# Optimization experiments

Hardware: AMD Instinct MI355X
Metric: run time of the kernel (lower is better)

Reference implementation:

```python
import jax, jax.numpy as jnp
import numpy as np

N_SAMPLES = 256   # n_samples from __init__
N_THIN = 10       # N from __init__
N_WORDS = 4096


def setup_inputs() -> dict:
    key = jax.random.key(0)
    k1, k2, k3 = jax.random.split(key, 3)
    # scale potentials so per-step weight deltas stay in a sane exp() range
    bigram = jax.random.normal(k1, (N_WORDS, N_WORDS), dtype=jnp.float32)
    start = jax.random.normal(k2, (N_WORDS,), dtype=jnp.float32)
    end = jax.random.normal(k3, (N_WORDS,), dtype=jnp.float32)
    return {"n_words": N_WORDS, "bigram": bigram, "start": start, "end": end}


def _mh_chain(bigram, start, end, n_words, chain_size, rng):
    # chain[0] = identity permutation (random_start=False)
    perm0 = jnp.arange(n_words, dtype=jnp.int32)
    w0 = bigram[perm0[:-1], perm0[1:]].sum() + start[perm0[0]] + end[perm0[-1]]

    def step(carry, k):
        perm, w_last = carry
        k_pos, k_cat, k_u = jax.random.split(k, 3)
        # pick a token to move, remove it -> perm2 of length n_words-1
        pos = jax.random.randint(k_pos, (), 0, n_words)
        to_move = perm[pos]
        j = jnp.arange(n_words - 1)
        perm2 = perm[j + (j >= pos).astype(j.dtype)]
        # insertion logits over n_words slots (self._probs, unnormalized log p)
        logits = jnp.zeros((n_words,), dtype=bigram.dtype)
        logits = logits.at[0].add(start[to_move]).at[-1].add(end[to_move])
        logits = logits.at[1:].add(bigram[perm2, to_move])   # left-neighbor term
        logits = logits.at[:-1].add(bigram[to_move, perm2])  # right-neighbor term
        p = jax.nn.softmax(logits)
        new_pos = jax.random.categorical(k_cat, logits)
        # insert to_move at new_pos
        jj = jnp.arange(n_words)
        shifted = perm2[jnp.clip(jj - (jj > new_pos).astype(jj.dtype), 0, n_words - 2)]
        sample = jnp.where(jj == new_pos, to_move, shifted).astype(perm.dtype)
        # new chain weight
        new_w = bigram[sample[:-1], sample[1:]].sum() + start[sample[0]] + end[sample[-1]]
        # MH accept ratio; removing to_move from sample recovers perm2, so the
        # reverse insertion distribution equals p -> ratio p[new_pos]/p[pos]
        acc = jnp.minimum(1.0, jnp.exp(new_w - w_last) * p[new_pos] / p[pos])
        accept = acc > jax.random.uniform(k_u, ())
        perm_next = jnp.where(accept, sample, perm)
        w_next = jnp.where(accept, new_w, w_last)
        return (perm_next, w_next), perm_next

    keys = jax.random.split(rng, chain_size - 1)
    _, perms = jax.lax.scan(step, (perm0, w0), keys)
    chain = jnp.concatenate([perm0[None, :], perms], axis=0)  # [chain_size, n_words]
    sel = jnp.arange(0, chain_size, N_THIN) + (N_THIN - 1)    # thin: every N-th state
    return chain[sel]


def reference(n_words, bigram, start, end):
    chain_size = N_SAMPLES * N_THIN
    rng = jax.random.key(42)
    return _mh_chain(bigram, start, end, n_words, chain_size, rng)
```

## Files before the change

### kernel.cpp

```cpp
#include <hip/hip_runtime.h>
#include <stdint.h>


#define NW 4096
#define NSTEPS 2559
#define NTHREADS 1024
#define NWAVES 16

typedef unsigned long long u64;
typedef uint32_t u32;
typedef unsigned short u16;

__device__ __forceinline__ u32 rotl32(u32 v, u32 r) { return (v << r) | (v >> (32u - r)); }

__device__ __forceinline__ void tf2x32(u32 k0, u32 k1, u32 x0, u32 x1, u32* o0, u32* o1) {
  u32 ks2 = k0 ^ k1 ^ 0x1BD11BDAu;
  x0 += k0; x1 += k1;
#define TFR(r0, r1, r2, r3)                      \
  x0 += x1; x1 = rotl32(x1, r0); x1 ^= x0;       \
  x0 += x1; x1 = rotl32(x1, r1); x1 ^= x0;       \
  x0 += x1; x1 = rotl32(x1, r2); x1 ^= x0;       \
  x0 += x1; x1 = rotl32(x1, r3); x1 ^= x0;
  TFR(13, 15, 26, 6)  x0 += k1;  x1 += ks2 + 1u;
  TFR(17, 29, 16, 24) x0 += ks2; x1 += k0 + 2u;
  TFR(13, 15, 26, 6)  x0 += k0;  x1 += k1 + 3u;
  TFR(17, 29, 16, 24) x0 += k1;  x1 += ks2 + 4u;
  TFR(13, 15, 26, 6)  x0 += ks2; x1 += k0 + 5u;
#undef TFR
  *o0 = x0; *o1 = x1;
}

__device__ __forceinline__ float unif01(u32 bits) {
  return __uint_as_float((bits >> 9) | 0x3f800000u) - 1.0f;
}

__device__ __forceinline__ u32 fkey(float f) {
  u32 b = __float_as_uint(f);
  return b ^ ((b >> 31) ? 0xFFFFFFFFu : 0x80000000u);
}

__device__ __forceinline__ void light_bar() {
  asm volatile("s_waitcnt lgkmcnt(0)" ::: "memory");
  __builtin_amdgcn_s_barrier();
  __builtin_amdgcn_sched_barrier(0);
  asm volatile("" ::: "memory");
}


template <int CTRL>
__device__ __forceinline__ u32 dpp32(u32 v) {
  return (u32)__builtin_amdgcn_update_dpp(0, (int)v, CTRL, 0xF, 0xF, true);
}

template <int CTRL>
__device__ __forceinline__ u32 dppumax(u32 v) {
  u32 s = dpp32<CTRL>(v);
  return (v > s) ? v : s;
}

template <int CTRL>
__device__ __forceinline__ void dppmax64(u32& hi, u32& lo) {
  u32 h2 = dpp32<CTRL>(hi);
  u32 l2 = dpp32<CTRL>(lo);
  bool g = (h2 > hi) || (h2 == hi && l2 > lo);
  hi = g ? h2 : hi;
  lo = g ? l2 : lo;
}

__device__ __forceinline__ u64 bfly16_max_u64(u64 key) {
  u32 lo = (u32)key, hi = (u32)(key >> 32);
  dppmax64<0xB1>(hi, lo); dppmax64<0x4E>(hi, lo);
  dppmax64<0x141>(hi, lo); dppmax64<0x140>(hi, lo);
  return ((u64)hi << 32) | lo;
}


#define TT 32
__global__ void transpose_k(const float* __restrict__ in, float* __restrict__ out) {
  __shared__ float tile[TT][TT + 1];
  int x = blockIdx.x * TT + threadIdx.x;
  int y = blockIdx.y * TT + threadIdx.y;
  for (int j = 0; j < TT; j += 8) tile[threadIdx.y + j][threadIdx.x] = in[(u64)(y + j) * NW + x];
  __syncthreads();
  x = blockIdx.y * TT + threadIdx.x;
  y = blockIdx.x * TT + threadIdx.y;
  for (int j = 0; j < TT; j += 8) out[(u64)(y + j) * NW + x] = tile[threadIdx.x][threadIdx.y + j];
}

__global__ void gumbel_k(float* __restrict__ gumb) {
  long long idx = (long long)blockIdx.x * blockDim.x + threadIdx.x;
  if (idx >= (long long)NSTEPS * NW) return;
  int t = (int)(idx >> 12);
  int i = (int)(idx & (NW - 1));
  u32 kt0, kt1, kc0, kc1, ba, bb;
  tf2x32(0u, 42u, 0u, (u32)t, &kt0, &kt1);
  tf2x32(kt0, kt1, 0u, 1u, &kc0, &kc1);
  tf2x32(kc0, kc1, 0u, (u32)i, &ba, &bb);
  float u = unif01(ba ^ bb);
  if (u == 0.0f) u = 1.17549435e-38f;
  float t1 = (float)log((double)u);
  float t2 = (float)log((double)(-t1));
  gumb[idx] = -t2;
}

__global__ void posu_k(int* __restrict__ posArr, float* __restrict__ uArr) {
  int t = blockIdx.x * blockDim.x + threadIdx.x;
  if (t >= NSTEPS) return;
  u32 kt0, kt1, kp0, kp1, ku0, ku1, k2a, k2b, ra, rb, ua, ub;
  tf2x32(0u, 42u, 0u, (u32)t, &kt0, &kt1);
  tf2x32(kt0, kt1, 0u, 0u, &kp0, &kp1);
  tf2x32(kt0, kt1, 0u, 2u, &ku0, &ku1);
  tf2x32(kp0, kp1, 0u, 1u, &k2a, &k2b);
  tf2x32(k2a, k2b, 0u, 0u, &ra, &rb);
  posArr[t] = (int)((ra ^ rb) & (u32)(NW - 1));
  tf2x32(ku0, ku1, 0u, 0u, &ua, &ub);
  uArr[t] = unif01(ua ^ ub);
}


#define SAMPLE_AT(idx)                                                        \
  ((idx) < np ? (int)s_perm[(idx) + ((idx) >= pos)]                           \
              : ((idx) == np ? tm                                             \
                             : (int)s_perm[((idx)-1) + (((idx)-1) >= pos)]))

__global__ __launch_bounds__(NTHREADS)
void mcmc_fast16(const float* __restrict__ bigram,
                 const float* __restrict__ bigT,
                 const float* __restrict__ gumb,
                 const int* __restrict__ posArr,
                 const float* __restrict__ uArr,
                 const float* __restrict__ startv,
                 const float* __restrict__ endv,
                 int* __restrict__ out) {
  __shared__ u16    s_perm[NW];
  __shared__ float  s_rowT[NW];
  __shared__ float  s_rowB[NW];
  __shared__ float  s_pairw[NW];
  __shared__ u64    s_redu[NWAVES];
  __shared__ float  s_stm, s_etm, s_lpos, s_brgS, s_vn1, s_vn2;
  __shared__ int    s_accs, s_tmA;

  const int tid = threadIdx.x;
  const int lane = tid & 63;
  const int wid = tid >> 6;
  const int j0 = tid * 4;

  for (int i = tid; i < NW; i += NTHREADS) s_perm[i] = (u16)i;
  ushort4 pq = make_ushort4((u16)j0, (u16)(j0 + 1), (u16)(j0 + 2), (u16)(j0 + 3));
  float4 pwq;
  pwq.x = bigram[(u64)j0 * NW + (j0 + 1)];
  pwq.y = bigram[(u64)(j0 + 1) * NW + (j0 + 2)];
  pwq.z = bigram[(u64)(j0 + 2) * NW + (j0 + 3)];
  pwq.w = (j0 + 3 < NW - 1) ? bigram[(u64)(j0 + 3) * NW + (j0 + 4)] : 0.0f;
  ((float4*)s_pairw)[tid] = pwq;

  int pos = posArr[0];
  int pn1 = posArr[1];
  float u_cur = uArr[0];
  float un1 = uArr[1];
  int tm = pos;
  {
    float4 rb4 = ((const float4*)(bigram + (u64)tm * NW))[tid];
    float4 rt4 = ((const float4*)(bigT + (u64)tm * NW))[tid];
    ((float4*)s_rowB)[tid] = rb4;
    ((float4*)s_rowT)[tid] = rt4;
  }
  if (tid == 0) { s_stm = startv[tm]; s_etm = endv[tm]; }

  float start_cur = startv[0];
  float end_cur = endv[NW - 1];

  float4 g4 = ((const float4*)gumb)[tid];
  __syncthreads();

  for (int t = 0; t < NSTEPS; ++t) {
    const float gg[4] = {g4.x, g4.y, g4.z, g4.w};
    const int tmR = (int)s_perm[pn1];
    const float4 rbR = ((const float4*)(bigram + (u64)tmR * NW))[tid];
    const float4 rtR = ((const float4*)(bigT + (u64)tmR * NW))[tid];
    float stmR = 0.0f, etmR = 0.0f;
    if (tid == 0) { stmR = startv[tmR]; etmR = endv[tmR]; }
    int pn2; float un2;
    {
      int tn = (t + 1 < NSTEPS) ? (t + 1) : (NSTEPS - 1);
      int tn2 = (t + 2 < NSTEPS) ? (t + 2) : (NSTEPS - 1);
      g4 = ((const float4*)(gumb + ((u64)tn << 12)))[tid];
      pn2 = posArr[tn2];
      un2 = uArr[tn2];
    }
    float stm_r = 0.0f, etm_r = 0.0f, remL = 0.0f, remR = 0.0f, brgv = 0.0f;
    float sv0m = 0.0f, ev1m = 0.0f;
    if (wid == 0) {
      stm_r = s_stm; etm_r = s_etm;
      int pl = (pos > 0) ? (int)s_perm[pos - 1] : 0;
      int pr = (pos < NW - 1) ? (int)s_perm[pos + 1] : 0;
      if (pos > 0)      remL = s_rowT[pl];
      if (pos < NW - 1) remR = s_rowB[pr];
      if (pos > 0 && pos < NW - 1) brgv = bigram[(u64)pl * NW + pr];
      sv0m = startv[(int)s_perm[(0 >= pos) ? 1 : 0]];
      ev1m = endv[(int)s_perm[(NW - 2) + ((NW - 2) >= pos)]];
      if (lane == 0) s_brgS = brgv;
    }

    const int p0i = pq.x, p1i = pq.y, p2i = pq.z, p3i = pq.w;
    int pm1, pp4;
    {
      u32 lo = (u32)pq.x | ((u32)pq.y << 16);
      u32 hi = (u32)pq.z | ((u32)pq.w << 16);
      pm1 = (int)(dpp32<0x138>(hi) >> 16);
      pp4 = (int)(dpp32<0x130>(lo) & 0xFFFFu);
      if (lane == 0)  pm1 = (tid > 0) ? (int)s_perm[j0 - 1] : 0;
      if (lane == 63) pp4 = (tid < NTHREADS - 1) ? (int)s_perm[j0 + 4] : 0;
    }
    float pwm1_e = 0.0f, pwp4_e = 0.0f;
    if (lane == 0 && tid > 0) pwm1_e = s_pairw[j0 - 1];
    if (lane == 63 && tid < NTHREADS - 1) pwp4_e = s_pairw[j0 + 4];

    const int w0 = (j0     >= pos) ? p1i : p0i;
    const int w1 = (j0 + 1 >= pos) ? p2i : p1i;
    const int w2 = (j0 + 2 >= pos) ? p3i : p2i;
    const int w3 = (j0 + 3 >= pos) ? pp4 : p3i;
    const int wprev = ((j0 - 1) >= pos) ? p0i : pm1;
    const float t0v = s_rowT[w0];
    const float t1v = s_rowT[w1];
    const float t2v = s_rowT[w2];
    const float t3v = s_rowT[w3];
    const float b0v = s_rowB[w0];
    const float b1v = s_rowB[w1];
    const float b2v = s_rowB[w2];
    const float b3v = s_rowB[w3];
    float tprev = __uint_as_float(dpp32<0x138>(__float_as_uint(t3v)));
    if (lane == 0 && tid > 0) tprev = s_rowT[wprev];
    float li0 = tprev + b0v;
    float li1 = t0v + b1v;
    float li2 = t1v + b2v;
    float li3 = t2v + b3v;
    if (tid == 0)            li0 = s_stm + b0v;
    if (tid == NTHREADS - 1) li3 = s_etm + t2v;
    if ((pos >> 2) == tid) {
      int k = pos & 3;
      s_lpos = (k == 0) ? li0 : ((k == 1) ? li1 : ((k == 2) ? li2 : li3));
    }
    {
      float sv0_ = gg[0] + li0;
      float sv1_ = gg[1] + li1;
      float sv2_ = gg[2] + li2;
      float sv3_ = gg[3] + li3;
      float mx = sv0_; int ix = j0;
      if (sv1_ > mx) { mx = sv1_; ix = j0 + 1; }
      if (sv2_ > mx) { mx = sv2_; ix = j0 + 2; }
      if (sv3_ > mx) { mx = sv3_; ix = j0 + 3; }
      u32 kloc = fkey(mx);
      u32 kr = kloc;
      kr = dppumax<0x111>(kr); kr = dppumax<0x112>(kr);
      kr = dppumax<0x114>(kr); kr = dppumax<0x118>(kr);
      kr = dppumax<0x142>(kr); kr = dppumax<0x143>(kr);
      u32 kmax = (u32)__builtin_amdgcn_readlane((int)kr, 63);
      u64 mask = __ballot(kloc == kmax);
      int wl = (int)(__ffsll((long long)mask)) - 1;
      if (lane == wl) s_redu[wid] = ((u64)kmax << 32) | (u32)(NW - 1 - ix);
    }
    light_bar();

    if (wid == 0) {
      u64 bb = bfly16_max_u64(s_redu[lane & 15]);
      const int np = NW - 1 - (int)(bb & 0xFFFFFFFFu);
      int ls_i = (np >= 1) ? ((np - 1) + ((np - 1) >= pos)) : 0;
      int rs_i = (np <= NW - 2) ? (np + (np >= pos)) : 0;
      const int l_s = (int)s_perm[ls_i];
      const int r_s = (int)s_perm[rs_i];
      const int tmA = SAMPLE_AT(pn1);
      float splitv = 0.0f;
      if (np > 0 && np < NW - 1) {
        int k_s = (np - 1) + ((np - 1) >= pos);
        splitv = (np == pos) ? brgv : s_pairw[k_s];
      }
      float vnpm1 = (np >= 1)      ? s_rowT[l_s] : 0.0f;
      float vnp   = (np <= NW - 2) ? s_rowB[r_s] : 0.0f;
      float sv0 = (np > 0) ? sv0m : stm_r;
      float ev1 = (np < NW - 1) ? ev1m : etm_r;
      float lposv = s_lpos;
      double delta = 0.0;
      if (pos > 0)                 delta -= (double)remL;
      if (pos < NW - 1)            delta -= (double)remR;
      if (pos > 0 && pos < NW - 1) delta += (double)brgv;
      if (np > 0)                  delta += (double)vnpm1;
      if (np < NW - 1)             delta += (double)vnp;
      if (np > 0 && np < NW - 1)   delta -= (double)splitv;
      delta += ((double)sv0 - (double)start_cur) + ((double)ev1 - (double)end_cur);
      float lnp = (np == 0) ? (stm_r + vnp)
                : ((np == NW - 1) ? (etm_r + vnpm1) : (vnpm1 + vnp));
      double ed = delta + ((double)lnp - (double)lposv);
      float a = fminf(1.0f, expf((float)ed));
      int acc = (a > u_cur) ? 1 : 0;
      if (lane == 0) { s_accs = acc; s_vn1 = vnpm1; s_vn2 = vnp; s_tmA = tmA; }
      if (acc) { start_cur = sv0; end_cur = ev1; }
    }
    light_bar();

    const int acc = s_accs;
    int tm_next = tmR;
    float4 rb = rbR, rt = rtR;
    ushort4 st = pq;
    if (acc) {
      tm_next = s_tmA;
      rb = ((const float4*)(bigram + (u64)tm_next * NW))[tid];
      rt = ((const float4*)(bigT + (u64)tm_next * NW))[tid];
      u64 bb = bfly16_max_u64(s_redu[lane & 15]);
      const int np = NW - 1 - (int)(bb & 0xFFFFFFFFu);
      st.x = (j0     < np) ? (u16)w0 : ((j0     == np) ? (u16)tm : (u16)wprev);
      st.y = (j0 + 1 < np) ? (u16)w1 : ((j0 + 1 == np) ? (u16)tm : (u16)w0);
      st.z = (j0 + 2 < np) ? (u16)w2 : ((j0 + 2 == np) ? (u16)tm : (u16)w1);
      st.w = (j0 + 3 < np) ? (u16)w3 : ((j0 + 3 == np) ? (u16)tm : (u16)w2);
      ((ushort4*)s_perm)[tid] = st;
      float pwm1 = __uint_as_float(dpp32<0x138>(__float_as_uint(pwq.w)));
      float pwp4 = __uint_as_float(dpp32<0x130>(__float_as_uint(pwq.x)));
      if (lane == 0)  pwm1 = pwm1_e;
      if (lane == 63) pwp4 = pwp4_e;
      const float brgAll = s_brgS;
      float nv0, nv1, nv2, nv3;
      {
        float vA0 = (j0     < pos - 1) ? pwq.x : pwq.y;
        float vB0 = (j0 - 1 < pos - 1) ? pwm1  : pwq.x;
        nv0 = (j0 < np) ? vA0 : vB0;
        int kk0 = (j0 < np) ? j0 : j0 - 1;
        if (kk0 == pos - 1) nv0 = brgAll;

        float vA1 = (j0 + 1 < pos - 1) ? pwq.y : pwq.z;
        float vB1 = (j0     < pos - 1) ? pwq.x : pwq.y;
        nv1 = (j0 + 1 < np) ? vA1 : vB1;
        int kk1 = (j0 + 1 < np) ? j0 + 1 : j0;
        if (kk1 == pos - 1) nv1 = brgAll;

        float vA2 = (j0 + 2 < pos - 1) ? pwq.z : pwq.w;
        float vB2 = (j0 + 1 < pos - 1) ? pwq.y : pwq.z;
        nv2 = (j0 + 2 < np) ? vA2 : vB2;
        int kk2 = (j0 + 2 < np) ? j0 + 2 : j0 + 1;
        if (kk2 == pos - 1) nv2 = brgAll;

        float vA3 = (j0 + 3 < pos - 1) ? pwq.w : pwp4;
        float vB3 = (j0 + 2 < pos - 1) ? pwq.z : pwq.w;
        nv3 = (j0 + 3 < np) ? vA3 : vB3;
        int kk3 = (j0 + 3 < np) ? j0 + 3 : j0 + 2;
        if (kk3 == pos - 1) nv3 = brgAll;
      }
      const float vn1 = s_vn1, vn2 = s_vn2;
      float o0 = (j0     == np - 1) ? vn1 : ((j0     == np) ? vn2 : nv0);
      float o1 = (j0 + 1 == np - 1) ? vn1 : ((j0 + 1 == np) ? vn2 : nv1);
      float o2 = (j0 + 2 == np - 1) ? vn1 : ((j0 + 2 == np) ? vn2 : nv2);
      float o3 = (j0 + 3 == np - 1) ? vn1 : ((j0 + 3 == np) ? vn2 : nv3);
      if (j0 + 3 >= NW - 1) o3 = 0.0f;
      pwq = make_float4(o0, o1, o2, o3);
      ((float4*)s_pairw)[tid] = pwq;
      if (tid == 0) { s_stm = startv[tm_next]; s_etm = endv[tm_next]; }
    } else {
      if (tid == 0) { s_stm = stmR; s_etm = etmR; }
    }
    ((float4*)s_rowB)[tid] = rb;
    ((float4*)s_rowT)[tid] = rt;
    pq = st;
    tm = tm_next;
    pos = pn1; u_cur = un1;
    pn1 = pn2; un1 = un2;

    if ((t % 10) == 8) {
      int row = (t - 8) / 10;
      int4 o4;
      o4.x = (int)pq.x; o4.y = (int)pq.y; o4.z = (int)pq.z; o4.w = (int)pq.w;
      ((int4*)(out + (u64)row * NW))[tid] = o4;
    }
    light_bar();
  }
}


__global__ __launch_bounds__(NTHREADS)
void mcmc_kernel(const float* __restrict__ bigram,
                 const float* __restrict__ startv,
                 const float* __restrict__ endv,
                 int* __restrict__ out) {
  __shared__ int    s_perm[NW];
  __shared__ float  s_logit[NW];
  __shared__ float  s_gath[NW];
  __shared__ float  s_redf[NWAVES];
  __shared__ u64    s_redu[NWAVES];
  __shared__ double s_redd[NWAVES];
  __shared__ float  s_m, s_Z, s_w;
  __shared__ int    s_pos, s_tm, s_np, s_acc;
  __shared__ u32    s_kcat0, s_kcat1, s_ku0, s_ku1;

  const int tid = threadIdx.x;
  const int lane = tid & 63;
  const int wid = tid >> 6;

  for (int i = tid; i < NW; i += NTHREADS) s_perm[i] = i;
  for (int j = tid; j < NW - 1; j += NTHREADS) s_gath[j] = bigram[(u64)j * NW + (j + 1)];
  __syncthreads();
  if (tid == 0) {
    float S = 0.0f;
    for (int j = 0; j < NW - 1; ++j) S += s_gath[j];
    S = S + startv[0];
    S = S + endv[NW - 1];
    s_w = S;
  }
  __syncthreads();

  for (int t = 0; t < NSTEPS; ++t) {
    if (tid == 0) {
      u32 kt0, kt1;
      tf2x32(0u, 42u, 0u, (u32)t, &kt0, &kt1);
      u32 kp0, kp1, kc0, kc1, ku0, ku1;
      tf2x32(kt0, kt1, 0u, 0u, &kp0, &kp1);
      tf2x32(kt0, kt1, 0u, 1u, &kc0, &kc1);
      tf2x32(kt0, kt1, 0u, 2u, &ku0, &ku1);
      u32 k2a, k2b, ra, rb;
      tf2x32(kp0, kp1, 0u, 1u, &k2a, &k2b);
      tf2x32(k2a, k2b, 0u, 0u, &ra, &rb);
      int pos = (int)((ra ^ rb) & (u32)(NW - 1));
      s_pos = pos;
      s_tm = s_perm[pos];
      s_kcat0 = kc0; s_kcat1 = kc1; s_ku0 = ku0; s_ku1 = ku1;
    }
    __syncthreads();
    const int pos = s_pos, tm = s_tm;

    float lmax = -3.402823466e+38f;
    for (int i = tid; i < NW; i += NTHREADS) {
      float li;
      if (i == 0) {
        int r = s_perm[(0 >= pos) ? 1 : 0];
        li = startv[tm] + bigram[(u64)tm * NW + r];
      } else if (i == NW - 1) {
        int l = s_perm[((NW - 2) >= pos) ? (NW - 1) : (NW - 2)];
        li = endv[tm] + bigram[(u64)l * NW + tm];
      } else {
        int l = s_perm[((i - 1) >= pos) ? i : (i - 1)];
        int r = s_perm[(i >= pos) ? (i + 1) : i];
        li = bigram[(u64)l * NW + tm] + bigram[(u64)tm * NW + r];
      }
      s_logit[i] = li;
      lmax = fmaxf(lmax, li);
    }
    for (int o = 32; o > 0; o >>= 1) lmax = fmaxf(lmax, __shfl_down(lmax, o, 64));
    if (lane == 0) s_redf[wid] = lmax;
    __syncthreads();
    if (tid == 0) {
      float m = s_redf[0];
      for (int w = 1; w < NWAVES; ++w) m = fmaxf(m, s_redf[w]);
      s_m = m;
    }
    __syncthreads();
    const float m = s_m;

    double zacc = 0.0;
    u64 best = 0;
    const u32 kc0 = s_kcat0, kc1 = s_kcat1;
    for (int i = tid; i < NW; i += NTHREADS) {
      float li = s_logit[i];
      float ex = (float)exp((double)(li - m));
      zacc += (double)ex;
      u32 ba, bb;
      tf2x32(kc0, kc1, 0u, (u32)i, &ba, &bb);
      float u = unif01(ba ^ bb);
      if (u == 0.0f) u = 1.17549435e-38f;
      float t1 = (float)log((double)u);
      float t2 = (float)log((double)(-t1));
      float g = -t2;
      float sv = g + li;
      u64 key = ((u64)fkey(sv) << 32) | (u32)(NW - 1 - i);
      if (key > best) best = key;
    }
    for (int o = 32; o > 0; o >>= 1) {
      u64 w = __shfl_down(best, o, 64);
      if (w > best) best = w;
      zacc += __shfl_down(zacc, o, 64);
    }
    if (lane == 0) { s_redu[wid] = best; s_redd[wid] = zacc; }
    __syncthreads();
    if (tid == 0) {
      u64 b = s_redu[0]; double z = s_redd[0];
      for (int w = 1; w < NWAVES; ++w) {
        if (s_redu[w] > b) b = s_redu[w];
        z += s_redd[w];
      }
      s_np = NW - 1 - (int)(b & 0xFFFFFFFFu);
      s_Z = (float)z;
    }
    __syncthreads();
    const int np = s_np;

    for (int j = tid; j < NW - 1; j += NTHREADS) {
      int a = (j < np) ? s_perm[j + (j >= pos)]
                       : ((j == np) ? tm : s_perm[(j - 1) + ((j - 1) >= pos)]);
      int j1 = j + 1;
      int b = (j1 < np) ? s_perm[j1 + (j1 >= pos)]
                        : ((j1 == np) ? tm : s_perm[(j1 - 1) + ((j1 - 1) >= pos)]);
      s_gath[j] = bigram[(u64)a * NW + b];
    }
    __syncthreads();

    if (tid == 0) {
      float S = 0.0f;
      for (int j = 0; j < NW - 1; ++j) S += s_gath[j];
      int s0 = (0 < np) ? s_perm[(0 >= pos) ? 1 : 0] : tm;
      int sl = ((NW - 1) == np) ? tm : s_perm[(NW - 2) + ((NW - 2) >= pos)];
      S = S + startv[s0];
      S = S + endv[sl];
      float dw = S - s_w;
      float e1 = (float)exp((double)dw);
      float en = (float)exp((double)(s_logit[np] - m));
      float eo = (float)exp((double)(s_logit[pos] - m));
      float pn = en / s_Z;
      float po = eo / s_Z;
      float acc = e1 * pn;
      acc = acc / po;
      acc = fminf(1.0f, acc);
      u32 ua, ub;
      tf2x32(s_ku0, s_ku1, 0u, 0u, &ua, &ub);
      float u = unif01(ua ^ ub);
      int accept = (acc > u) ? 1 : 0;
      s_acc = accept;
      if (accept) s_w = S;
    }
    __syncthreads();

    int stash[4];
    if (s_acc) {
      for (int k = 0; k < 4; ++k) {
        int i = tid + k * NTHREADS;
        stash[k] = (i < np) ? s_perm[i + (i >= pos)]
                            : ((i == np) ? tm : s_perm[(i - 1) + ((i - 1) >= pos)]);
      }
    }
    __syncthreads();
    if (s_acc) {
      for (int k = 0; k < 4; ++k) {
        int i = tid + k * NTHREADS;
        s_perm[i] = stash[k];
      }
    }
    __syncthreads();

    if (((t + 1) % 10) == 9) {
      int row = (t - 8) / 10;
      for (int i = tid; i < NW; i += NTHREADS) out[(u64)row * NW + i] = s_perm[i];
    }
    __syncthreads();
  }
}

extern "C" void kernel_launch(void* const* d_in, const int* in_sizes, int n_in,
                              void* d_out, int out_size, void* d_ws, size_t ws_size,
                              hipStream_t stream) {
  const float* bigram = (const float*)d_in[1];
  const float* startv = (const float*)d_in[2];
  const float* endv   = (const float*)d_in[3];
  int* out = (int*)d_out;

  const size_t needT = (size_t)NW * NW * sizeof(float);
  const size_t needG = (size_t)NSTEPS * NW * sizeof(float);
  const size_t needP = (size_t)NSTEPS * (sizeof(int) + sizeof(float));

  if (ws_size >= needT + needG + needP) {
    float* bigT = (float*)d_ws;
    float* gumb = (float*)((char*)d_ws + needT);
    int* posArr = (int*)((char*)d_ws + needT + needG);
    float* uArr = (float*)((char*)d_ws + needT + needG + (size_t)NSTEPS * sizeof(int));
    hipLaunchKernelGGL(transpose_k, dim3(NW / TT, NW / TT), dim3(TT, 8), 0, stream,
                       bigram, bigT);
    long long ng = (long long)NSTEPS * NW;
    hipLaunchKernelGGL(gumbel_k, dim3((unsigned)((ng + 255) / 256)), dim3(256), 0, stream,
                       gumb);
    hipLaunchKernelGGL(posu_k, dim3((NSTEPS + 255) / 256), dim3(256), 0, stream,
                       posArr, uArr);
    hipLaunchKernelGGL(mcmc_fast16, dim3(1), dim3(NTHREADS), 0, stream,
                       bigram, bigT, gumb, posArr, uArr, startv, endv, out);
  } else {
    hipLaunchKernelGGL(mcmc_kernel, dim3(1), dim3(NTHREADS), 0, stream,
                       bigram, startv, endv, out);
  }
}
```

Before: 6.496 ms.

## Double-buffer gathered row tiles and skip end-of-step barrier on reject

Splits the shared bigram row/column buffers into two copies that alternate each step. The speculative next row is written into the spare buffer right after the mid-step barrier, and the trailing barrier now runs only when a proposal is accepted and the buffers must be overwritten. The start/end potentials for the moved token also move from shared scalars into per-thread registers. Together these aim to drop one block-wide barrier per step on the common reject path, in exchange for twice the shared memory for rows and more complex ordering reasoning around buffer reuse.

```diff
diff --git a/kernel.cpp b/kernel.cpp
--- a/kernel.cpp
+++ b/kernel.cpp
@@ -124,7 +124,7 @@
                              : (int)s_perm[((idx)-1) + (((idx)-1) >= pos)]))
 
 __global__ __launch_bounds__(NTHREADS)
-void mcmc_fast16(const float* __restrict__ bigram,
+void mcmc_fast17(const float* __restrict__ bigram,
                  const float* __restrict__ bigT,
                  const float* __restrict__ gumb,
                  const int* __restrict__ posArr,
@@ -133,17 +133,18 @@
                  const float* __restrict__ endv,
                  int* __restrict__ out) {
   __shared__ u16    s_perm[NW];
-  __shared__ float  s_rowT[NW];
-  __shared__ float  s_rowB[NW];
+  __shared__ float  s_rowT[2][NW];
+  __shared__ float  s_rowB[2][NW];
   __shared__ float  s_pairw[NW];
   __shared__ u64    s_redu[NWAVES];
-  __shared__ float  s_stm, s_etm, s_lpos, s_brgS, s_vn1, s_vn2;
+  __shared__ float  s_lpos, s_brgS, s_vn1, s_vn2;
   __shared__ int    s_accs, s_tmA;
 
   const int tid = threadIdx.x;
   const int lane = tid & 63;
   const int wid = tid >> 6;
   const int j0 = tid * 4;
+  int cur = 0;
 
   for (int i = tid; i < NW; i += NTHREADS) s_perm[i] = (u16)i;
   ushort4 pq = make_ushort4((u16)j0, (u16)(j0 + 1), (u16)(j0 + 2), (u16)(j0 + 3));
@@ -162,11 +163,11 @@
   {
     float4 rb4 = ((const float4*)(bigram + (u64)tm * NW))[tid];
     float4 rt4 = ((const float4*)(bigT + (u64)tm * NW))[tid];
-    ((float4*)s_rowB)[tid] = rb4;
-    ((float4*)s_rowT)[tid] = rt4;
+    ((float4*)s_rowB[0])[tid] = rb4;
+    ((float4*)s_rowT[0])[tid] = rt4;
   }
-  if (tid == 0) { s_stm = startv[tm]; s_etm = endv[tm]; }
-
+  float stm_cur = startv[tm];
+  float etm_cur = endv[tm];
   float start_cur = startv[0];
   float end_cur = endv[NW - 1];
 
@@ -174,12 +175,15 @@
   __syncthreads();
 
   for (int t = 0; t < NSTEPS; ++t) {
+    const float* rowT = s_rowT[cur];
+    const float* rowB = s_rowB[cur];
+
     const float gg[4] = {g4.x, g4.y, g4.z, g4.w};
     const int tmR = (int)s_perm[pn1];
     const float4 rbR = ((const float4*)(bigram + (u64)tmR * NW))[tid];
     const float4 rtR = ((const float4*)(bigT + (u64)tmR * NW))[tid];
-    float stmR = 0.0f, etmR = 0.0f;
-    if (tid == 0) { stmR = startv[tmR]; etmR = endv[tmR]; }
+    const float stmR = startv[tmR];
+    const float etmR = endv[tmR];
     int pn2; float un2;
     {
       int tn = (t + 1 < NSTEPS) ? (t + 1) : (NSTEPS - 1);
@@ -188,14 +192,12 @@
       pn2 = posArr[tn2];
       un2 = uArr[tn2];
     }
-    float stm_r = 0.0f, etm_r = 0.0f, remL = 0.0f, remR = 0.0f, brgv = 0.0f;
-    float sv0m = 0.0f, ev1m = 0.0f;
+    float remL = 0.0f, remR = 0.0f, brgv = 0.0f, sv0m = 0.0f, ev1m = 0.0f;
     if (wid == 0) {
-      stm_r = s_stm; etm_r = s_etm;
       int pl = (pos > 0) ? (int)s_perm[pos - 1] : 0;
       int pr = (pos < NW - 1) ? (int)s_perm[pos + 1] : 0;
-      if (pos > 0)      remL = s_rowT[pl];
-      if (pos < NW - 1) remR = s_rowB[pr];
+      if (pos > 0)      remL = rowT[pl];
+      if (pos < NW - 1) remR = rowB[pr];
       if (pos > 0 && pos < NW - 1) brgv = bigram[(u64)pl * NW + pr];
       sv0m = startv[(int)s_perm[(0 >= pos) ? 1 : 0]];
       ev1m = endv[(int)s_perm[(NW - 2) + ((NW - 2) >= pos)]];
@@ -221,22 +223,22 @@
     const int w2 = (j0 + 2 >= pos) ? p3i : p2i;
     const int w3 = (j0 + 3 >= pos) ? pp4 : p3i;
     const int wprev = ((j0 - 1) >= pos) ? p0i : pm1;
-    const float t0v = s_rowT[w0];
-    const float t1v = s_rowT[w1];
-    const float t2v = s_rowT[w2];
-    const float t3v = s_rowT[w3];
-    const float b0v = s_rowB[w0];
-    const float b1v = s_rowB[w1];
-    const float b2v = s_rowB[w2];
-    const float b3v = s_rowB[w3];
+    const float t0v = rowT[w0];
+    const float t1v = rowT[w1];
+    const float t2v = rowT[w2];
+    const float t3v = rowT[w3];
+    const float b0v = rowB[w0];
+    const float b1v = rowB[w1];
+    const float b2v = rowB[w2];
+    const float b3v = rowB[w3];
     float tprev = __uint_as_float(dpp32<0x138>(__float_as_uint(t3v)));
-    if (lane == 0 && tid > 0) tprev = s_rowT[wprev];
+    if (lane == 0 && tid > 0) tprev = rowT[wprev];
     float li0 = tprev + b0v;
     float li1 = t0v + b1v;
     float li2 = t1v + b2v;
     float li3 = t2v + b3v;
-    if (tid == 0)            li0 = s_stm + b0v;
-    if (tid == NTHREADS - 1) li3 = s_etm + t2v;
+    if (tid == 0)            li0 = stm_cur + b0v;
+    if (tid == NTHREADS - 1) li3 = etm_cur + t2v;
     if ((pos >> 2) == tid) {
       int k = pos & 3;
       s_lpos = (k == 0) ? li0 : ((k == 1) ? li1 : ((k == 2) ? li2 : li3));
@@ -262,6 +264,8 @@
     }
     light_bar();
 
+    ((float4*)s_rowB[cur ^ 1])[tid] = rbR;
+    ((float4*)s_rowT[cur ^ 1])[tid] = rtR;
     if (wid == 0) {
       u64 bb = bfly16_max_u64(s_redu[lane & 15]);
       const int np = NW - 1 - (int)(bb & 0xFFFFFFFFu);
@@ -275,10 +279,10 @@
         int k_s = (np - 1) + ((np - 1) >= pos);
         splitv = (np == pos) ? brgv : s_pairw[k_s];
       }
-      float vnpm1 = (np >= 1)      ? s_rowT[l_s] : 0.0f;
-      float vnp   = (np <= NW - 2) ? s_rowB[r_s] : 0.0f;
-      float sv0 = (np > 0) ? sv0m : stm_r;
-      float ev1 = (np < NW - 1) ? ev1m : etm_r;
+      float vnpm1 = (np >= 1)      ? rowT[l_s] : 0.0f;
+      float vnp   = (np <= NW - 2) ? rowB[r_s] : 0.0f;
+      float sv0 = (np > 0) ? sv0m : stm_cur;
+      float ev1 = (np < NW - 1) ? ev1m : etm_cur;
       float lposv = s_lpos;
       double delta = 0.0;
       if (pos > 0)                 delta -= (double)remL;
@@ -288,8 +292,8 @@
       if (np < NW - 1)             delta += (double)vnp;
       if (np > 0 && np < NW - 1)   delta -= (double)splitv;
       delta += ((double)sv0 - (double)start_cur) + ((double)ev1 - (double)end_cur);
-      float lnp = (np == 0) ? (stm_r + vnp)
-                : ((np == NW - 1) ? (etm_r + vnpm1) : (vnpm1 + vnp));
+      float lnp = (np == 0) ? (stm_cur + vnp)
+                : ((np == NW - 1) ? (etm_cur + vnpm1) : (vnpm1 + vnp));
       double ed = delta + ((double)lnp - (double)lposv);
       float a = fminf(1.0f, expf((float)ed));
       int acc = (a > u_cur) ? 1 : 0;
@@ -300,12 +304,14 @@
 
     const int acc = s_accs;
     int tm_next = tmR;
-    float4 rb = rbR, rt = rtR;
+    float stmN = stmR, etmN = etmR;
     ushort4 st = pq;
     if (acc) {
       tm_next = s_tmA;
-      rb = ((const float4*)(bigram + (u64)tm_next * NW))[tid];
-      rt = ((const float4*)(bigT + (u64)tm_next * NW))[tid];
+      const float4 rbA = ((const float4*)(bigram + (u64)tm_next * NW))[tid];
+      const float4 rtA = ((const float4*)(bigT + (u64)tm_next * NW))[tid];
+      stmN = startv[tm_next];
+      etmN = endv[tm_next];
       u64 bb = bfly16_max_u64(s_redu[lane & 15]);
       const int np = NW - 1 - (int)(bb & 0xFFFFFFFFu);
       st.x = (j0     < np) ? (u16)w0 : ((j0     == np) ? (u16)tm : (u16)wprev);
@@ -352,16 +358,16 @@
       if (j0 + 3 >= NW - 1) o3 = 0.0f;
       pwq = make_float4(o0, o1, o2, o3);
       ((float4*)s_pairw)[tid] = pwq;
-      if (tid == 0) { s_stm = startv[tm_next]; s_etm = endv[tm_next]; }
-    } else {
-      if (tid == 0) { s_stm = stmR; s_etm = etmR; }
-    }
-    ((float4*)s_rowB)[tid] = rb;
-    ((float4*)s_rowT)[tid] = rt;
+      ((float4*)s_rowB[cur ^ 1])[tid] = rbA;
+      ((float4*)s_rowT[cur ^ 1])[tid] = rtA;
+    }
+    cur ^= 1;
     pq = st;
+    stm_cur = stmN; etm_cur = etmN;
     tm = tm_next;
     pos = pn1; u_cur = un1;
     pn1 = pn2; un1 = un2;
+    if (acc) light_bar();
 
     if ((t % 10) == 8) {
       int row = (t - 8) / 10;
@@ -369,7 +375,6 @@
       o4.x = (int)pq.x; o4.y = (int)pq.y; o4.z = (int)pq.z; o4.w = (int)pq.w;
       ((int4*)(out + (u64)row * NW))[tid] = o4;
     }
-    light_bar();
   }
 }
 
@@ -573,7 +578,7 @@
                        gumb);
     hipLaunchKernelGGL(posu_k, dim3((NSTEPS + 255) / 256), dim3(256), 0, stream,
                        posArr, uArr);
-    hipLaunchKernelGGL(mcmc_fast16, dim3(1), dim3(NTHREADS), 0, stream,
+    hipLaunchKernelGGL(mcmc_fast17, dim3(1), dim3(NTHREADS), 0, stream,
                        bigram, bigT, gumb, posArr, uArr, startv, endv, out);
   } else {
     hipLaunchKernelGGL(mcmc_kernel, dim3(1), dim3(NTHREADS), 0, stream,
```

Result: no change. 6.388 ms (-1.7%).
